# Kernel optimization log

Measured on AMD Instinct MI355X. Metric: run time of the kernel, lower is better.

## Reference

```python
import jax, jax.numpy as jnp
import numpy as np

NUM_CLASSES = 250
NUM_EMB = 128
EMB_DIM = 512
HID = 256
IN_DIM = 225
COMMIT = 0.25


def _lstm_dir(x, Wih, Whh, b, reverse):
    # x: [B, T, D]; Wih: [4H, D]; Whh: [4H, H]; b: [4H]
    B = x.shape[0]
    H = Whh.shape[1]
    xs = jnp.swapaxes(x, 0, 1)            # [T, B, D]
    pre = xs @ Wih.T + b                   # precompute input projection: [T, B, 4H]

    def step(carry, pre_t):
        h, c = carry
        g = pre_t + h @ Whh.T
        i, f, gg, o = jnp.split(g, 4, axis=-1)  # torch gate order i,f,g,o
        i = jax.nn.sigmoid(i)
        f = jax.nn.sigmoid(f)
        gg = jnp.tanh(gg)
        o = jax.nn.sigmoid(o)
        c = f * c + i * gg
        h = o * jnp.tanh(c)
        return (h, c), h

    init = (jnp.zeros((B, H), x.dtype), jnp.zeros((B, H), x.dtype))
    _, hs = jax.lax.scan(step, init, pre, reverse=reverse)
    return jnp.swapaxes(hs, 0, 1)          # [B, T, H]


def _bilstm(x, Wih_f, Whh_f, b_f, Wih_b, Whh_b, b_b):
    hf = _lstm_dir(x, Wih_f, Whh_f, b_f, reverse=False)
    hb = _lstm_dir(x, Wih_b, Whh_b, b_b, reverse=True)
    return jnp.concatenate([hf, hb], axis=-1)  # [B, T, 2H]


def _vq(z, codebook):
    flat = z.reshape(-1, codebook.shape[1])  # [N, E]
    d = (jnp.sum(flat ** 2, axis=1, keepdims=True)
         + jnp.sum(codebook ** 2, axis=1)
         - 2.0 * flat @ codebook.T)          # [N, K]
    idx = jnp.argmin(d, axis=1)              # [N]
    q = codebook[idx].reshape(z.shape)
    e_loss = jnp.mean((jax.lax.stop_gradient(q) - z) ** 2)
    q_loss = jnp.mean((q - jax.lax.stop_gradient(z)) ** 2)
    loss = q_loss + COMMIT * e_loss
    q_st = z + jax.lax.stop_gradient(q - z)  # straight-through
    return q_st, loss


def setup_inputs() -> dict:
    key = jax.random.key(0)
    ks = jax.random.split(key, 16)
    s = 0.05
    d = {
        'x': jax.random.normal(ks[0], (64, 512, IN_DIM), dtype=jnp.float32),
        'enc_Wih_f': jax.random.normal(ks[1], (4 * HID, IN_DIM), jnp.float32) * s,
        'enc_Whh_f': jax.random.normal(ks[2], (4 * HID, HID), jnp.float32) * s,
        'enc_b_f': jnp.zeros((4 * HID,), jnp.float32),
        'enc_Wih_b': jax.random.normal(ks[3], (4 * HID, IN_DIM), jnp.float32) * s,
        'enc_Whh_b': jax.random.normal(ks[4], (4 * HID, HID), jnp.float32) * s,
        'enc_b_b': jnp.zeros((4 * HID,), jnp.float32),
        'codebook': jax.random.uniform(ks[5], (NUM_EMB, EMB_DIM), jnp.float32,
                                       minval=-1.0 / NUM_EMB, maxval=1.0 / NUM_EMB),
        'dec_Wih_f': jax.random.normal(ks[6], (4 * HID, EMB_DIM), jnp.float32) * s,
        'dec_Whh_f': jax.random.normal(ks[7], (4 * HID, HID), jnp.float32) * s,
        'dec_b_f': jnp.zeros((4 * HID,), jnp.float32),
        'dec_Wih_b': jax.random.normal(ks[8], (4 * HID, EMB_DIM), jnp.float32) * s,
        'dec_Whh_b': jax.random.normal(ks[9], (4 * HID, HID), jnp.float32) * s,
        'dec_b_b': jnp.zeros((4 * HID,), jnp.float32),
        'W_cls': jax.random.normal(ks[10], (NUM_CLASSES, EMB_DIM), jnp.float32) * s,
        'b_cls': jnp.zeros((NUM_CLASSES,), jnp.float32),
    }
    return d


def reference(x, enc_Wih_f, enc_Whh_f, enc_b_f, enc_Wih_b, enc_Whh_b, enc_b_b,
              codebook, dec_Wih_f, dec_Whh_f, dec_b_f, dec_Wih_b, dec_Whh_b, dec_b_b,
              W_cls, b_cls):
    enc_out = _bilstm(x, enc_Wih_f, enc_Whh_f, enc_b_f, enc_Wih_b, enc_Whh_b, enc_b_b)  # [B,T,512]
    quantized, vq_loss = _vq(enc_out, codebook)
    dec_out = _bilstm(quantized, dec_Wih_f, dec_Whh_f, dec_b_f, dec_Wih_b, dec_Whh_b, dec_b_b)
    logits = dec_out[:, -1] @ W_cls.T + b_cls  # [B, num_classes]
    return logits, vq_loss
```

## Files before the change

### kernel.cpp

```cpp
#include <hip/hip_runtime.h>
#include <hip/hip_fp16.h>
#include <cstddef>

#define Bb 64
#define Tt 512
#define INRAW 225
#define Hh 256
#define G4 1024
#define Ee 512
#define NCODE 128
#define NCLS 250

typedef _Float16 half8_t __attribute__((ext_vector_type(8)));
typedef _Float16 half4_t __attribute__((ext_vector_type(4)));
typedef float f32x4 __attribute__((ext_vector_type(4)));
typedef unsigned u32x4 __attribute__((ext_vector_type(4)));

__device__ __forceinline__ float sigf(float x) { return 1.0f / (1.0f + expf(-x)); }
__device__ __forceinline__ float fsig(float x) { return __builtin_amdgcn_rcpf(1.0f + __expf(-x)); }
__device__ __forceinline__ float ftanh(float x) {
  return 2.0f * __builtin_amdgcn_rcpf(1.0f + __expf(-2.0f * x)) - 1.0f;
}

__device__ __forceinline__ unsigned pkmax16(unsigned a, unsigned b) {
  unsigned r;
  asm("v_pk_max_i16 %0, %1, %2" : "=v"(r) : "v"(a), "v"(b));
  return r;
}

__global__ __launch_bounds__(256) void prep_all_k(
    u32x4* __restrict__ hexfill,
    const float* __restrict__ x, _Float16* __restrict__ xh,
    const float* __restrict__ cb,
    const float* __restrict__ dWihF, const float* __restrict__ dbF,
    _Float16* __restrict__ projFh,
    const float* __restrict__ dWihB, const float* __restrict__ dbB,
    float* __restrict__ projBf,
    const float* __restrict__ eWhhF, _Float16* __restrict__ wphF,
    const float* __restrict__ eWhhB, _Float16* __restrict__ wphB,
    const float* __restrict__ dWhhF, _Float16* __restrict__ wphD,
    const float* __restrict__ eWihF, _Float16* __restrict__ wpihF,
    const float* __restrict__ eWihB, _Float16* __restrict__ wpihB) {
  int blk = blockIdx.x;
  const int tid = threadIdx.x;

  if (blk < 12288) {
    long i = (long)blk * 256 + tid;
    u32x4 sv = {0x7C007C00u, 0x7C007C00u, 0x7C007C00u, 0x7C007C00u};
    asm volatile("global_store_dwordx4 %0, %1, off sc0 sc1"
                 :: "v"(hexfill + i), "v"(sv) : "memory");
    return;
  }
  blk -= 12288;
  if (blk < 32768) {
    int idx = blk * 256 + tid;
    int row = idx >> 8, k = idx & 255;
    xh[idx] = (k < INRAW) ? (_Float16)x[(size_t)row * INRAW + k] : (_Float16)0.f;
    return;
  }
  blk -= 32768;
  if (blk < 512) {
    int n = (blk & 3) * 256 + tid;
    int code = blk >> 2;
    const float4* cr = (const float4*)(cb + (size_t)code * Ee);
    const float4* wr = (const float4*)(dWihF + (size_t)n * Ee);
    float acc = 0.f;
#pragma unroll 4
    for (int e4 = 0; e4 < Ee / 4; ++e4) {
      float4 cv = cr[e4], wv = wr[e4];
      acc = fmaf(cv.x, wv.x, acc); acc = fmaf(cv.y, wv.y, acc);
      acc = fmaf(cv.z, wv.z, acc); acc = fmaf(cv.w, wv.w, acc);
    }
    int g = n >> 8, u = n & 255;
    projFh[(size_t)code * 1024 + u * 4 + g] = (_Float16)(acc + dbF[n]);
    return;
  }
  blk -= 512;
  if (blk < 512) {
    int n = (blk & 3) * 256 + tid;
    int code = blk >> 2;
    const float4* cr = (const float4*)(cb + (size_t)code * Ee);
    const float4* wr = (const float4*)(dWihB + (size_t)n * Ee);
    float acc = 0.f;
#pragma unroll 4
    for (int e4 = 0; e4 < Ee / 4; ++e4) {
      float4 cv = cr[e4], wv = wr[e4];
      acc = fmaf(cv.x, wv.x, acc); acc = fmaf(cv.y, wv.y, acc);
      acc = fmaf(cv.z, wv.z, acc); acc = fmaf(cv.w, wv.w, acc);
    }
    projBf[(size_t)code * 1024 + n] = acc + dbB[n];
    return;
  }
  blk -= 512;
  if (blk < 3072) {
    const float* W = (blk < 1024) ? eWhhF : (blk < 2048) ? eWhhB : dWhhF;
    _Float16* wp = (blk < 1024) ? wphF : (blk < 2048) ? wphB : wphD;
    int idx = (blk & 1023) * 256 + tid;
    int e = idx & 7, l = (idx >> 3) & 63, zg = (idx >> 9) & 7;
    int ks = (idx >> 12) & 7, wv = (idx >> 15) & 7;
    int z = zg >> 2, g = zg & 3;
    int u = wv * 32 + z * 16 + (l & 15);
    int k = ks * 32 + (l >> 4) * 8 + e;
    wp[idx] = (_Float16)W[(size_t)(g * 256 + u) * 256 + k];
    return;
  }
  blk -= 3072;
  {
    const float* W = (blk < 1024) ? eWihF : eWihB;
    _Float16* wp = (blk < 1024) ? wpihF : wpihB;
    int idx = (blk & 1023) * 256 + tid;
    int e = idx & 7, l = (idx >> 3) & 63;
    int tail = idx >> 9;
    int ks = tail & 7; tail >>= 3;
    int z = tail & 1, w = (tail >> 1) & 7, g = tail >> 4;
    if (g >= 4) return;
    int k = ks * 32 + (l >> 4) * 8 + e;
    int u = w * 32 + z * 16 + (l & 15);
    wp[idx] = (k < INRAW) ? (_Float16)W[(size_t)(g * 256 + u) * INRAW + k] : (_Float16)0.f;
  }
}

__global__ __launch_bounds__(256) void gemm_mfma_pre(const _Float16* __restrict__ Ah,
                                                     const _Float16* __restrict__ Bp0,
                                                     const float* __restrict__ bias0,
                                                     __half* __restrict__ C0,
                                                     const _Float16* __restrict__ Bp1,
                                                     const float* __restrict__ bias1,
                                                     __half* __restrict__ C1, int K) {
  const int t = blockIdx.x, g = blockIdx.y;
  const int zsel = blockIdx.z;
  const _Float16* Bp = zsel ? Bp1 : Bp0;
  const float* bias = zsel ? bias1 : bias0;
  __half* C = zsel ? C1 : C0;
  const int bg = threadIdx.x >> 6;
  const int l = threadIdx.x & 63, l15 = l & 15, lg = l >> 4;
  const int KS = K >> 5;

  f32x4 acc[16];
#pragma unroll
  for (int ct = 0; ct < 16; ++ct) acc[ct] = (f32x4){0.f, 0.f, 0.f, 0.f};

  const _Float16* arow = Ah + ((size_t)(bg * 16 + l15) * 512 + t) * K + lg * 8;

  for (int kh = 0; kh < KS; kh += 8) {
    half8_t af[8];
#pragma unroll
    for (int k2 = 0; k2 < 8; ++k2)
      af[k2] = *(const half8_t*)(arow + (kh + k2) * 32);
#pragma unroll
    for (int ct = 0; ct < 16; ++ct) {
      const int w = ct >> 1, z = ct & 1;
      const _Float16* bb = Bp + ((((size_t)(g * 8 + w) * 2 + z) * KS + kh) * 64 + l) * 8;
#pragma unroll
      for (int k2 = 0; k2 < 8; ++k2) {
        half8_t bf = *(const half8_t*)(bb + (size_t)k2 * 512);
        acc[ct] = __builtin_amdgcn_mfma_f32_16x16x32_f16(af[k2], bf, acc[ct], 0, 0, 0);
      }
    }
  }

#pragma unroll
  for (int ct = 0; ct < 16; ++ct) {
    const int w = ct >> 1, z = ct & 1;
    const int u = w * 32 + z * 16 + l15;
    const float bs = bias[g * 256 + u];
    union { unsigned short us[4]; uint2 u2; } pk;
#pragma unroll
    for (int j = 0; j < 4; ++j) {
      __half hv = __float2half(acc[ct][j] + bs);
      pk.us[j] = *(unsigned short*)&hv;
    }
    __half* dst = C + ((((size_t)t * 4 + bg) * 8 + w) * 2 + z) * 1024 + l * 16 + g * 4;
    *(uint2*)dst = pk.u2;
  }
}

__global__ __launch_bounds__(64) void lstm_scan_sync(
    const half8_t* __restrict__ preF, const half8_t* __restrict__ wF,
    _Float16* __restrict__ hexF,
    const half8_t* __restrict__ preB, const half8_t* __restrict__ wB,
    _Float16* __restrict__ hexB, int nfwd) {
  const int isB = (blockIdx.x >= nfwd) ? 1 : 0;
  const half8_t* pre = isB ? preB : preF;
  const half8_t* wfrag = isB ? wB : wF;
  _Float16* hex = isB ? hexB : hexF;
  const int bid = blockIdx.x - (isB ? nfwd : 0);
  const int rg = bid >> 4, sl = bid & 15;
  const int w_ = sl >> 1, z_ = sl & 1;
  const int l = threadIdx.x, l15 = l & 15, lg = l >> 4;
  const int u0 = sl * 16;

  half8_t bfr[8][4];
#pragma unroll
  for (int ks = 0; ks < 8; ++ks)
#pragma unroll
    for (int g = 0; g < 4; ++g)
      bfr[ks][g] = wfrag[(size_t)((w_ * 8 + ks) * 8 + z_ * 4 + g) * 64 + l];

  float c[4] = {0.f, 0.f, 0.f, 0.f};
  half8_t pc0, pc1;
  {
    const int t0 = isB ? (Tt - 1) : 0;
    const half8_t* pp = pre + ((size_t)(t0 * 4 + rg) * 16 + sl) * 128 + l * 2;
    pc0 = pp[0]; pc1 = pp[1];
  }

  for (int s = 0; s < Tt; ++s) {
    f32x4 acc[4];
#pragma unroll
    for (int g = 0; g < 4; ++g)
#pragma unroll
      for (int j = 0; j < 4; ++j)
        acc[g][j] = (float)((g < 2 ? pc0 : pc1)[(g & 1) * 4 + j]);

    if (s + 1 < Tt) {
      const int tn = isB ? (Tt - 2 - s) : (s + 1);
      const half8_t* pp = pre + ((size_t)(tn * 4 + rg) * 16 + sl) * 128 + l * 2;
      pc0 = pp[0]; pc1 = pp[1];
    }

    if (s > 0) {
      const char* ab = (const char*)hex + (((size_t)(s - 1) * 64 + rg * 16) * 256) * 2;
      half8_t afr[8];
      while (true) {
#pragma unroll
        for (int ks = 0; ks < 8; ++ks) {
          const void* ap = (const void*)(ab + l15 * 512 + ks * 64 + lg * 16);
          asm volatile("global_load_dwordx4 %0, %1, off sc0 sc1"
                       : "=v"(afr[ks]) : "v"(ap) : "memory");
        }
        asm volatile("s_waitcnt vmcnt(0)" ::: "memory");
        union HU { half8_t h; u32x4 u; } cu;
        cu.h = afr[0];
        unsigned mm = pkmax16(pkmax16(cu.u[0], cu.u[1]), pkmax16(cu.u[2], cu.u[3]));
#pragma unroll
        for (int ks = 1; ks < 8; ++ks) {
          cu.h = afr[ks];
          mm = pkmax16(mm, pkmax16(pkmax16(cu.u[0], cu.u[1]), pkmax16(cu.u[2], cu.u[3])));
        }
        int bad = ((mm & 0xFFFFu) == 0x7C00u) || ((mm >> 16) == 0x7C00u);
        if (__all(!bad)) break;
      }
      __builtin_amdgcn_sched_barrier(0);

#pragma unroll
      for (int ks = 0; ks < 8; ++ks)
#pragma unroll
        for (int g = 0; g < 4; ++g)
          acc[g] = __builtin_amdgcn_mfma_f32_16x16x32_f16(afr[ks], bfr[ks][g], acc[g], 0, 0, 0);
    }

#pragma unroll
    for (int j = 0; j < 4; ++j) {
      float iv = fsig(acc[0][j]);
      float fv = fsig(acc[1][j]);
      float gv = ftanh(acc[2][j]);
      float ov = fsig(acc[3][j]);
      c[j] = fv * c[j] + iv * gv;
      float hv = ov * ftanh(c[j]);
      union { _Float16 f; unsigned short u; } cv;
      cv.f = (_Float16)hv;
      unsigned hb32 = cv.u;
      const void* hp = (const void*)(hex + ((size_t)s * 64 + rg * 16 + lg * 4 + j) * 256
                                     + u0 + l15);
      asm volatile("global_store_short %0, %1, off sc0 sc1"
                   :: "v"(hp), "v"(hb32) : "memory");
    }
  }
}

#define VPB 4
__global__ __launch_bounds__(128) void vq_kernel(const _Float16* __restrict__ hexF,
                                                 const _Float16* __restrict__ hexB,
                                                 const float* __restrict__ cb,
                                                 int* __restrict__ idxOut,
                                                 float* __restrict__ dmin) {
  const int tid = threadIdx.x;
  const int v0 = blockIdx.x * VPB;
  __shared__ __align__(16) float zs[VPB][Ee];
  __shared__ float dsh[NCODE];
  __shared__ int ish[NCODE];

#pragma unroll
  for (int v = 0; v < VPB; ++v) {
    const int vv = v0 + v;
    const int b = vv >> 9, t = vv & 511;
    const _Float16* hf = hexF + ((size_t)t * 64 + b) * 256;
    const _Float16* hb = hexB + ((size_t)(Tt - 1 - t) * 64 + b) * 256;
    zs[v][tid]       = (float)hf[tid];
    zs[v][tid + 128] = (float)hf[tid + 128];
    zs[v][tid + 256] = (float)hb[tid];
    zs[v][tid + 384] = (float)hb[tid + 128];
  }
  __syncthreads();

  float dv[VPB] = {0.0f, 0.0f, 0.0f, 0.0f};
  const float4* crow = (const float4*)(cb + (size_t)tid * Ee);
#pragma unroll 2
  for (int e4 = 0; e4 < Ee / 4; ++e4) {
    float4 cc = crow[e4];
#pragma unroll
    for (int v = 0; v < VPB; ++v) {
      float4 z = *(const float4*)&zs[v][e4 * 4];
      float t0 = z.x - cc.x, t1 = z.y - cc.y, t2 = z.z - cc.z, t3 = z.w - cc.w;
      dv[v] = fmaf(t0, t0, dv[v]);
      dv[v] = fmaf(t1, t1, dv[v]);
      dv[v] = fmaf(t2, t2, dv[v]);
      dv[v] = fmaf(t3, t3, dv[v]);
    }
  }

#pragma unroll
  for (int v = 0; v < VPB; ++v) {
    __syncthreads();
    dsh[tid] = dv[v];
    ish[tid] = tid;
    __syncthreads();
    for (int off = 64; off > 0; off >>= 1) {
      if (tid < off) {
        float dn = dsh[tid + off];
        int in_ = ish[tid + off];
        if (dn < dsh[tid] || (dn == dsh[tid] && in_ < ish[tid])) {
          dsh[tid] = dn;
          ish[tid] = in_;
        }
      }
      __syncthreads();
    }
    if (tid == 0) {
      idxOut[v0 + v] = ish[0];
      dmin[v0 + v] = dsh[0];
    }
  }
}

__global__ __launch_bounds__(256) void gather_pre_k(const int* __restrict__ idx,
                                                    const _Float16* __restrict__ projFh,
                                                    __half* __restrict__ C) {
  const int t = blockIdx.x;
  const int b_ = threadIdx.x >> 6;
  const int l = threadIdx.x & 63, l15 = l & 15, lg = l >> 4;

  int cj[4];
#pragma unroll
  for (int j = 0; j < 4; ++j)
    cj[j] = idx[(size_t)(b_ * 16 + lg * 4 + j) * 512 + t];

#pragma unroll
  for (int w_ = 0; w_ < 8; ++w_) {
#pragma unroll
    for (int z_ = 0; z_ < 2; ++z_) {
      const int u = w_ * 32 + z_ * 16 + l15;
      half4_t pv[4];
#pragma unroll
      for (int j = 0; j < 4; ++j)
        pv[j] = *(const half4_t*)(projFh + (size_t)cj[j] * 1024 + u * 4);
      union { _Float16 h[16]; u32x4 q[2]; } outv;
#pragma unroll
      for (int g = 0; g < 4; ++g)
#pragma unroll
        for (int j = 0; j < 4; ++j)
          outv.h[g * 4 + j] = pv[j][g];
      __half* dst = C + ((((size_t)t * 4 + b_) * 8 + w_) * 2 + z_) * 1024 + l * 16;
      *(u32x4*)dst = outv.q[0];
      *(u32x4*)(dst + 8) = outv.q[1];
    }
  }
}

__global__ __launch_bounds__(1024) void vq_reduce(const float* __restrict__ dmin,
                                                  float* __restrict__ out) {
  __shared__ float sh[1024];
  int tid = threadIdx.x;
  float s = 0.0f;
  for (int i = tid; i < Bb * Tt; i += 1024) s += dmin[i];
  sh[tid] = s;
  __syncthreads();
  for (int off = 512; off > 0; off >>= 1) {
    if (tid < off) sh[tid] += sh[tid + off];
    __syncthreads();
  }
  if (tid == 0) out[Bb * NCLS] = sh[0] * (1.25f / ((float)(Bb * Tt) * (float)Ee));
}

__global__ __launch_bounds__(256) void dec_bwd_last(const int* __restrict__ idx,
                                                    const float* __restrict__ projBf,
                                                    float* __restrict__ hb_last) {
  int b = blockIdx.x, tid = threadIdx.x;
  const int c = idx[(size_t)b * 512 + 511];
  const float* pr = projBf + (size_t)c * 1024;
  float a0 = pr[tid], a1 = pr[256 + tid], a2 = pr[512 + tid], a3 = pr[768 + tid];
  float i = sigf(a0), f = sigf(a1), g = tanhf(a2), o = sigf(a3);
  (void)f;
  float cc = i * g;
  hb_last[b * Hh + tid] = o * tanhf(cc);
}

__global__ __launch_bounds__(256) void classifier_k(const _Float16* __restrict__ hexD,
                                                    const float* __restrict__ hb_last,
                                                    const float* __restrict__ Wcls,
                                                    const float* __restrict__ bcls,
                                                    float* __restrict__ out) {
  int b = blockIdx.x, tid = threadIdx.x;
  __shared__ __align__(16) float dl[Ee];
  dl[tid] = (float)hexD[((size_t)(Tt - 1) * 64 + b) * 256 + tid];
  dl[tid + 256] = hb_last[b * Hh + tid];
  __syncthreads();
  if (tid < NCLS) {
    const float4* wr = (const float4*)(Wcls + (size_t)tid * Ee);
    float acc = bcls[tid];
#pragma unroll 4
    for (int e4 = 0; e4 < Ee / 4; ++e4) {
      float4 w = wr[e4];
      float4 z = *(const float4*)&dl[e4 * 4];
      acc = fmaf(w.x, z.x, acc);
      acc = fmaf(w.y, z.y, acc);
      acc = fmaf(w.z, z.z, acc);
      acc = fmaf(w.w, z.w, acc);
    }
    out[b * NCLS + tid] = acc;
  }
}

extern "C" void kernel_launch(void* const* d_in, const int* in_sizes, int n_in,
                              void* d_out, int out_size, void* d_ws, size_t ws_size,
                              hipStream_t stream) {
  const float* x     = (const float*)d_in[0];
  const float* eWihF = (const float*)d_in[1];
  const float* eWhhF = (const float*)d_in[2];
  const float* ebF   = (const float*)d_in[3];
  const float* eWihB = (const float*)d_in[4];
  const float* eWhhB = (const float*)d_in[5];
  const float* ebB   = (const float*)d_in[6];
  const float* cb    = (const float*)d_in[7];
  const float* dWihF = (const float*)d_in[8];
  const float* dWhhF = (const float*)d_in[9];
  const float* dbF   = (const float*)d_in[10];
  const float* dWihB = (const float*)d_in[11];
  const float* dbB   = (const float*)d_in[13];
  const float* Wcls  = (const float*)d_in[14];
  const float* bcls  = (const float*)d_in[15];
  float* out = (float*)d_out;
  float* w = (float*)d_ws;

  const size_t MR = (size_t)Bb * Tt;
  const size_t SZ_PRE_H = MR * G4 / 2;
  const size_t SZ_HEX  = (size_t)Tt * Bb * Hh / 2;
  const size_t SZ_XH   = MR * 256 / 2;
  const size_t SZ_WPH  = (size_t)G4 * Hh / 2;
  const size_t SZ_WIH  = (size_t)4 * 8 * 2 * 8 * 64 * 8 / 2;
  const size_t SZ_PJF  = (size_t)NCODE * G4 / 2;
  const size_t SZ_PJB  = (size_t)NCODE * G4;

  size_t o = 0;
  __half* preFh = (__half*)(w + o); o += SZ_PRE_H;
  __half* preBh = (__half*)(w + o); o += SZ_PRE_H;
  _Float16* hexF = (_Float16*)(w + o); o += SZ_HEX;
  _Float16* hexB = (_Float16*)(w + o); o += SZ_HEX;
  _Float16* hexD = (_Float16*)(w + o); o += SZ_HEX;
  _Float16* xh = (_Float16*)(w + o); o += SZ_XH;
  _Float16* wphF = (_Float16*)(w + o); o += SZ_WPH;
  _Float16* wphB = (_Float16*)(w + o); o += SZ_WPH;
  _Float16* wphD = (_Float16*)(w + o); o += SZ_WPH;
  _Float16* wpihF = (_Float16*)(w + o); o += SZ_WIH;
  _Float16* wpihB = (_Float16*)(w + o); o += SZ_WIH;
  _Float16* projFh = (_Float16*)(w + o); o += SZ_PJF;
  float* projBf = w + o; o += SZ_PJB;
  int* idxp = (int*)(w + o); o += MR;
  float* dminp = w + o; o += MR;
  float* hbl   = w + o; o += (size_t)Bb * Hh;
  __half* dprf = preBh;

  hipLaunchKernelGGL(prep_all_k, dim3(51200), dim3(256), 0, stream,
                     (u32x4*)hexF, x, xh,
                     cb, dWihF, dbF, projFh, dWihB, dbB, projBf,
                     eWhhF, wphF, eWhhB, wphB, dWhhF, wphD,
                     eWihF, wpihF, eWihB, wpihB);

  hipLaunchKernelGGL(gemm_mfma_pre, dim3(Tt, 4, 2), dim3(256), 0, stream,
                     xh, wpihF, ebF, preFh, wpihB, ebB, preBh, 256);

  hipLaunchKernelGGL(lstm_scan_sync, dim3(128), dim3(64), 0, stream,
                     (const half8_t*)preFh, (const half8_t*)wphF, hexF,
                     (const half8_t*)preBh, (const half8_t*)wphB, hexB, 64);

  hipLaunchKernelGGL(vq_kernel, dim3((int)(MR / VPB)), dim3(128), 0, stream,
                     hexF, hexB, cb, idxp, dminp);
  hipLaunchKernelGGL(vq_reduce, dim3(1), dim3(1024), 0, stream, dminp, out);

  hipLaunchKernelGGL(gather_pre_k, dim3(Tt), dim3(256), 0, stream,
                     idxp, projFh, dprf);

  hipLaunchKernelGGL(dec_bwd_last, dim3(Bb), dim3(256), 0, stream, idxp, projBf, hbl);

  hipLaunchKernelGGL(lstm_scan_sync, dim3(64), dim3(64), 0, stream,
                     (const half8_t*)dprf, (const half8_t*)wphD, hexD,
                     (const half8_t*)dprf, (const half8_t*)wphD, hexD, 64);

  hipLaunchKernelGGL(classifier_k, dim3(Bb), dim3(256), 0, stream,
                     hexD, hbl, Wcls, bcls, out);
}
```

Before: 2.399 ms.

## Fuse decoder input gather into LSTM scan via LDS-resident projection table

The separate gather kernel that materialized the decoder's per-timestep gate pre-activations is removed. The decoder scan now loads the code indices and the 128-code projection slice into LDS, and looks up the pre-activation each step instead of streaming a large precomputed buffer from global memory. The backward-last-step computation is folded into the classifier kernel, saving a launch. The cost is about 32KB of LDS per block for indices plus a per-step LDS lookup on the serial critical path.

```diff
diff --git a/kernel.cpp b/kernel.cpp
--- a/kernel.cpp
+++ b/kernel.cpp
@@ -269,6 +269,102 @@
   }
 }
 
+__global__ __launch_bounds__(64) void lstm_scan_dec(
+    const int* __restrict__ idx, const _Float16* __restrict__ projFh,
+    const half8_t* __restrict__ wfrag, _Float16* __restrict__ hex) {
+  const int bid = blockIdx.x;
+  const int rg = bid >> 4, sl = bid & 15;
+  const int w_ = sl >> 1, z_ = sl & 1;
+  const int l = threadIdx.x, l15 = l & 15, lg = l >> 4;
+  const int u0 = sl * 16;
+
+  __shared__ int idx_sh[16][512];
+  __shared__ __align__(8) _Float16 proj_sh[NCODE][16][4];
+
+  for (int i = l; i < 16 * 512; i += 64) {
+    int r = i >> 9, t = i & 511;
+    idx_sh[r][t] = idx[(size_t)(rg * 16 + r) * 512 + t];
+  }
+  for (int i = l; i < NCODE * 16; i += 64) {
+    int code = i >> 4, uu = i & 15;
+    *(half4_t*)&proj_sh[code][uu][0] =
+        *(const half4_t*)(projFh + (size_t)code * 1024 + (u0 + uu) * 4);
+  }
+
+  half8_t bfr[8][4];
+#pragma unroll
+  for (int ks = 0; ks < 8; ++ks)
+#pragma unroll
+    for (int g = 0; g < 4; ++g)
+      bfr[ks][g] = wfrag[(size_t)((w_ * 8 + ks) * 8 + z_ * 4 + g) * 64 + l];
+
+  __syncthreads();
+
+  float c[4] = {0.f, 0.f, 0.f, 0.f};
+
+  for (int s = 0; s < Tt; ++s) {
+    half4_t pv[4];
+#pragma unroll
+    for (int j = 0; j < 4; ++j)
+      pv[j] = *(const half4_t*)&proj_sh[idx_sh[lg * 4 + j][s]][l15][0];
+
+    f32x4 acc[4];
+#pragma unroll
+    for (int g = 0; g < 4; ++g)
+#pragma unroll
+      for (int j = 0; j < 4; ++j)
+        acc[g][j] = (float)pv[j][g];
+
+    if (s > 0) {
+      const char* ab = (const char*)hex + (((size_t)(s - 1) * 64 + rg * 16) * 256) * 2;
+      half8_t afr[8];
+      while (true) {
+#pragma unroll
+        for (int ks = 0; ks < 8; ++ks) {
+          const void* ap = (const void*)(ab + l15 * 512 + ks * 64 + lg * 16);
+          asm volatile("global_load_dwordx4 %0, %1, off sc0 sc1"
+                       : "=v"(afr[ks]) : "v"(ap) : "memory");
+        }
+        asm volatile("s_waitcnt vmcnt(0)" ::: "memory");
+        union HU { half8_t h; u32x4 u; } cu;
+        cu.h = afr[0];
+        unsigned mm = pkmax16(pkmax16(cu.u[0], cu.u[1]), pkmax16(cu.u[2], cu.u[3]));
+#pragma unroll
+        for (int ks = 1; ks < 8; ++ks) {
+          cu.h = afr[ks];
+          mm = pkmax16(mm, pkmax16(pkmax16(cu.u[0], cu.u[1]), pkmax16(cu.u[2], cu.u[3])));
+        }
+        int bad = ((mm & 0xFFFFu) == 0x7C00u) || ((mm >> 16) == 0x7C00u);
+        if (__all(!bad)) break;
+      }
+      __builtin_amdgcn_sched_barrier(0);
+
+#pragma unroll
+      for (int ks = 0; ks < 8; ++ks)
+#pragma unroll
+        for (int g = 0; g < 4; ++g)
+          acc[g] = __builtin_amdgcn_mfma_f32_16x16x32_f16(afr[ks], bfr[ks][g], acc[g], 0, 0, 0);
+    }
+
+#pragma unroll
+    for (int j = 0; j < 4; ++j) {
+      float iv = fsig(acc[0][j]);
+      float fv = fsig(acc[1][j]);
+      float gv = ftanh(acc[2][j]);
+      float ov = fsig(acc[3][j]);
+      c[j] = fv * c[j] + iv * gv;
+      float hv = ov * ftanh(c[j]);
+      union { _Float16 f; unsigned short u; } cv;
+      cv.f = (_Float16)hv;
+      unsigned hb32 = cv.u;
+      const void* hp = (const void*)(hex + ((size_t)s * 64 + rg * 16 + lg * 4 + j) * 256
+                                     + u0 + l15);
+      asm volatile("global_store_short %0, %1, off sc0 sc1"
+                   :: "v"(hp), "v"(hb32) : "memory");
+    }
+  }
+}
+
 #define VPB 4
 __global__ __launch_bounds__(128) void vq_kernel(const _Float16* __restrict__ hexF,
                                                  const _Float16* __restrict__ hexB,
@@ -334,40 +430,6 @@
   }
 }
 
-__global__ __launch_bounds__(256) void gather_pre_k(const int* __restrict__ idx,
-                                                    const _Float16* __restrict__ projFh,
-                                                    __half* __restrict__ C) {
-  const int t = blockIdx.x;
-  const int b_ = threadIdx.x >> 6;
-  const int l = threadIdx.x & 63, l15 = l & 15, lg = l >> 4;
-
-  int cj[4];
-#pragma unroll
-  for (int j = 0; j < 4; ++j)
-    cj[j] = idx[(size_t)(b_ * 16 + lg * 4 + j) * 512 + t];
-
-#pragma unroll
-  for (int w_ = 0; w_ < 8; ++w_) {
-#pragma unroll
-    for (int z_ = 0; z_ < 2; ++z_) {
-      const int u = w_ * 32 + z_ * 16 + l15;
-      half4_t pv[4];
-#pragma unroll
-      for (int j = 0; j < 4; ++j)
-        pv[j] = *(const half4_t*)(projFh + (size_t)cj[j] * 1024 + u * 4);
-      union { _Float16 h[16]; u32x4 q[2]; } outv;
-#pragma unroll
-      for (int g = 0; g < 4; ++g)
-#pragma unroll
-        for (int j = 0; j < 4; ++j)
-          outv.h[g * 4 + j] = pv[j][g];
-      __half* dst = C + ((((size_t)t * 4 + b_) * 8 + w_) * 2 + z_) * 1024 + l * 16;
-      *(u32x4*)dst = outv.q[0];
-      *(u32x4*)(dst + 8) = outv.q[1];
-    }
-  }
-}
-
 __global__ __launch_bounds__(1024) void vq_reduce(const float* __restrict__ dmin,
                                                   float* __restrict__ out) {
   __shared__ float sh[1024];
@@ -383,28 +445,23 @@
   if (tid == 0) out[Bb * NCLS] = sh[0] * (1.25f / ((float)(Bb * Tt) * (float)Ee));
 }
 
-__global__ __launch_bounds__(256) void dec_bwd_last(const int* __restrict__ idx,
+__global__ __launch_bounds__(256) void classifier_k(const _Float16* __restrict__ hexD,
+                                                    const int* __restrict__ idx,
                                                     const float* __restrict__ projBf,
-                                                    float* __restrict__ hb_last) {
-  int b = blockIdx.x, tid = threadIdx.x;
-  const int c = idx[(size_t)b * 512 + 511];
-  const float* pr = projBf + (size_t)c * 1024;
-  float a0 = pr[tid], a1 = pr[256 + tid], a2 = pr[512 + tid], a3 = pr[768 + tid];
-  float i = sigf(a0), f = sigf(a1), g = tanhf(a2), o = sigf(a3);
-  (void)f;
-  float cc = i * g;
-  hb_last[b * Hh + tid] = o * tanhf(cc);
-}
-
-__global__ __launch_bounds__(256) void classifier_k(const _Float16* __restrict__ hexD,
-                                                    const float* __restrict__ hb_last,
                                                     const float* __restrict__ Wcls,
                                                     const float* __restrict__ bcls,
                                                     float* __restrict__ out) {
   int b = blockIdx.x, tid = threadIdx.x;
   __shared__ __align__(16) float dl[Ee];
   dl[tid] = (float)hexD[((size_t)(Tt - 1) * 64 + b) * 256 + tid];
-  dl[tid + 256] = hb_last[b * Hh + tid];
+  {
+    const int c = idx[(size_t)b * 512 + 511];
+    const float* pr = projBf + (size_t)c * 1024;
+    float a0 = pr[tid], a1 = pr[256 + tid], a2 = pr[512 + tid], a3 = pr[768 + tid];
+    float i = sigf(a0), g = tanhf(a2), o = sigf(a3);
+    (void)a1;
+    dl[tid + 256] = o * tanhf(i * g);
+  }
   __syncthreads();
   if (tid < NCLS) {
     const float4* wr = (const float4*)(Wcls + (size_t)tid * Ee);
@@ -468,8 +525,6 @@
   float* projBf = w + o; o += SZ_PJB;
   int* idxp = (int*)(w + o); o += MR;
   float* dminp = w + o; o += MR;
-  float* hbl   = w + o; o += (size_t)Bb * Hh;
-  __half* dprf = preBh;
 
   hipLaunchKernelGGL(prep_all_k, dim3(51200), dim3(256), 0, stream,
                      (u32x4*)hexF, x, xh,
@@ -488,15 +543,9 @@
                      hexF, hexB, cb, idxp, dminp);
   hipLaunchKernelGGL(vq_reduce, dim3(1), dim3(1024), 0, stream, dminp, out);
 
-  hipLaunchKernelGGL(gather_pre_k, dim3(Tt), dim3(256), 0, stream,
-                     idxp, projFh, dprf);
-
-  hipLaunchKernelGGL(dec_bwd_last, dim3(Bb), dim3(256), 0, stream, idxp, projBf, hbl);
-
-  hipLaunchKernelGGL(lstm_scan_sync, dim3(64), dim3(64), 0, stream,
-                     (const half8_t*)dprf, (const half8_t*)wphD, hexD,
-                     (const half8_t*)dprf, (const half8_t*)wphD, hexD, 64);
+  hipLaunchKernelGGL(lstm_scan_dec, dim3(64), dim3(64), 0, stream,
+                     idxp, projFh, (const half8_t*)wphD, hexD);
 
   hipLaunchKernelGGL(classifier_k, dim3(Bb), dim3(256), 0, stream,
-                     hexD, hbl, Wcls, bcls, out);
-}
+                     hexD, idxp, projBf, Wcls, bcls, out);
+}
```

Result: slower. 2.474 ms (+3.2%).
